# Kernel optimization log

Hardware: AMD Instinct MI355X
Metric: run time of the kernel (lower is better)

The kernel has to match this reference:

```python
import jax, jax.numpy as jnp
import numpy as np

NCLUSTERS = 256


def setup_inputs() -> dict:
    key = jax.random.key(0)
    k1, k2 = jax.random.split(key)
    pr = jax.random.normal(k1, (1024, 16384), dtype=jnp.float32)
    vr = jax.random.randint(k2, (1024, 16384, 1), 0, NCLUSTERS, dtype=jnp.int32)
    return {"pr": pr, "vr": vr}


def _group_score(pr, vr):
    nc = NCLUSTERS
    v2d = jnp.squeeze(vr, -1)            # [B, S] int cluster ids
    p = pr.reshape(-1)                   # [N]
    v = v2d.reshape(-1)                  # [N]

    # segmented mean / min / max over clusters (fused segment reduce)
    counts = jax.ops.segment_sum(jnp.ones_like(p), v, num_segments=nc)
    sums = jax.ops.segment_sum(p, v, num_segments=nc)
    vmeans = sums / counts               # empty cluster -> 0/0 = nan (matches TF)
    vmins = jax.ops.segment_min(p, v, num_segments=nc)
    vmaxs = jax.ops.segment_max(p, v, num_segments=nc)

    no_scale = vmins == vmaxs            # [nc]
    vmins_g = jnp.where(no_scale, 0.0, vmins)[v2d]   # [B, S]
    vmaxs_g = jnp.where(no_scale, 1.0, vmaxs)[v2d]   # [B, S]

    # replace nan means (empty clusters) by min(valid)/2
    nan_idx = jnp.isnan(vmeans)
    valid_min = jnp.min(jnp.where(nan_idx, jnp.inf, vmeans))
    vmeans = jnp.where(nan_idx, valid_min * 0.5, vmeans)

    # sort means, smooth with 2-tap conv, unsort
    sort_ids = jnp.argsort(vmeans)
    orig_ids = jnp.argsort(sort_ids)
    vm_s = vmeans[sort_ids]
    conv_data = jnp.concatenate([vm_s[:1], vm_s, vm_s[-1:] * 2.0])   # [nc+2]
    pair = conv_data[:-1] + conv_data[1:]                            # [nc+1]
    f0 = (pair / 1.99)[:-1]   # f0[i] = (vm_s[i-1]+vm_s[i])/1.99 (edge-padded)
    f1 = (pair / 2.01)[1:]    # f1[i] = (vm_s[i]+vm_s[i+1])/2.01, last uses 2*vm_s[-1]
    f0_g = jnp.where(no_scale, 0.0, f0[orig_ids])[v2d]  # [B, S]
    f1_g = jnp.where(no_scale, 1.0, f1[orig_ids])[v2d]  # [B, S]

    sg = jax.lax.stop_gradient
    tmp = (sg(pr) - sg(vmins_g)) / sg(vmaxs_g - vmins_g) * sg(f1_g - f0_g) + sg(f0_g)
    scale = pr / tmp
    scale = jnp.where(jnp.isnan(scale) | jnp.isinf(scale), 0.0, scale)
    return pr * sg(scale)                # [B, S]


def reference(pr, vr):
    return _group_score(pr, vr)
```

## Files before the change

### kernel.cpp

```cpp
#include <hip/hip_runtime.h>
#include <math.h>


constexpr int NC   = 256;
constexpr int TILE = 16384;


__device__ __forceinline__ unsigned int map_f(float f) {
    unsigned int u = __float_as_uint(f);
    return ((int)u < 0) ? ~u : (u | 0x80000000u);
}
__device__ __forceinline__ float unmap_f(unsigned int u) {
    return __uint_as_float((u & 0x80000000u) ? (u & 0x7FFFFFFFu) : ~u);
}

__global__ __launch_bounds__(256) void init_k(unsigned* __restrict__ g_mn,
                                              unsigned* __restrict__ g_mx) {
    g_mn[threadIdx.x] = 0xFFFFFFFFu;
    g_mx[threadIdx.x] = 0u;
}

__global__ __launch_bounds__(256) void count_k(const float* __restrict__ pr,
                                               const int* __restrict__ vr,
                                               unsigned* __restrict__ tileCnt,
                                               unsigned* __restrict__ g_mn,
                                               unsigned* __restrict__ g_mx) {
    __shared__ unsigned s_cnt[NC];
    __shared__ unsigned s_mn[NC];
    __shared__ unsigned s_mx[NC];
    const int t = blockIdx.x;
    const int tid = threadIdx.x;
    s_cnt[tid] = 0u; s_mn[tid] = 0xFFFFFFFFu; s_mx[tid] = 0u;
    __syncthreads();

    const int4*   vr4 = (const int4*)(vr) + t * (TILE / 4);
    const float4* pr4 = (const float4*)(pr) + t * (TILE / 4);
    #pragma unroll
    for (int it = 0; it < TILE / 1024; ++it) {
        int4   v = vr4[it * 256 + tid];
        float4 p = pr4[it * 256 + tid];
        int c0 = v.x & 255, c1 = v.y & 255, c2 = v.z & 255, c3 = v.w & 255;
        atomicAdd(&s_cnt[c0], 1u); atomicAdd(&s_cnt[c1], 1u);
        atomicAdd(&s_cnt[c2], 1u); atomicAdd(&s_cnt[c3], 1u);
        unsigned u0 = map_f(p.x), u1 = map_f(p.y), u2 = map_f(p.z), u3 = map_f(p.w);
        atomicMin(&s_mn[c0], u0); atomicMax(&s_mx[c0], u0);
        atomicMin(&s_mn[c1], u1); atomicMax(&s_mx[c1], u1);
        atomicMin(&s_mn[c2], u2); atomicMax(&s_mx[c2], u2);
        atomicMin(&s_mn[c3], u3); atomicMax(&s_mx[c3], u3);
    }
    __syncthreads();
    tileCnt[t * NC + tid] = s_cnt[tid];
    if (s_mn[tid] != 0xFFFFFFFFu) {
        atomicMin(&g_mn[tid], s_mn[tid]);
        atomicMax(&g_mx[tid], s_mx[tid]);
    }
}

__global__ __launch_bounds__(256) void colscan_k(unsigned* __restrict__ tileCnt,
                                                 int nt,
                                                 unsigned* __restrict__ cnt) {
    __shared__ unsigned th_sum[256];
    __shared__ unsigned ex[257];
    const int c = blockIdx.x;
    const int tid = threadIdx.x;
    const int per = nt / 256;
    unsigned loc[8];
    unsigned run = 0;
    for (int k = 0; k < per; ++k) {
        loc[k] = tileCnt[(tid * per + k) * NC + c];
        run += loc[k];
    }
    th_sum[tid] = run;
    __syncthreads();
    if (tid == 0) {
        unsigned a = 0;
        for (int j = 0; j < 256; ++j) { ex[j] = a; a += th_sum[j]; }
        ex[256] = a;
    }
    __syncthreads();
    unsigned r2 = ex[tid];
    for (int k = 0; k < per; ++k) {
        unsigned x = loc[k];
        tileCnt[(tid * per + k) * NC + c] = r2;
        r2 += x;
    }
    if (tid == 0) cnt[c] = ex[256];
}

__global__ __launch_bounds__(64) void base_k(const unsigned* __restrict__ cnt,
                                             unsigned* __restrict__ baseArr) {
    if (threadIdx.x == 0) {
        unsigned a = 0;
        for (int j = 0; j < NC; ++j) { baseArr[j] = a; a += cnt[j]; }
    }
}

__global__ __launch_bounds__(256) void scatter_k(const float* __restrict__ pr,
                                                 const int* __restrict__ vr,
                                                 const unsigned* __restrict__ tilePre,
                                                 const unsigned* __restrict__ baseArr,
                                                 float* __restrict__ srt) {
    constexpr int NW = 4;
    constexpr int QT = TILE / NW;
    __shared__ float bins[TILE];
    __shared__ unsigned whist[NW][NC];
    __shared__ unsigned wcur[NW][NC];
    __shared__ unsigned binStart[NC + 1];
    const int t = blockIdx.x;
    const int tid = threadIdx.x;
    const int w = tid >> 6, lane = tid & 63;

    for (int j = tid; j < NW * NC; j += 256) ((unsigned*)whist)[j] = 0u;
    __syncthreads();

    const int qbase = t * TILE + w * QT;
    const int4* vq4 = (const int4*)(vr + qbase);
    for (int i = lane; i < QT / 4; i += 64) {
        int4 v = vq4[i];
        atomicAdd(&whist[w][v.x & 255], 1u);
        atomicAdd(&whist[w][v.y & 255], 1u);
        atomicAdd(&whist[w][v.z & 255], 1u);
        atomicAdd(&whist[w][v.w & 255], 1u);
    }
    __syncthreads();

    {
        const int c = tid;
        unsigned off = 0;
        #pragma unroll
        for (int ww = 0; ww < NW; ++ww) {
            unsigned x = whist[ww][c];
            whist[ww][c] = off;
            off += x;
        }
        binStart[c] = off;
    }
    __syncthreads();
    if (tid == 0) {
        unsigned a = 0;
        for (int j = 0; j < NC; ++j) { unsigned x = binStart[j]; binStart[j] = a; a += x; }
        binStart[NC] = a;
    }
    __syncthreads();
    {
        const int c = tid;
        #pragma unroll
        for (int ww = 0; ww < NW; ++ww) wcur[ww][c] = binStart[c] + whist[ww][c];
    }
    __syncthreads();

    for (int g = 0; g < QT / 64; ++g) {
        int idx = qbase + g * 64 + lane;
        int v   = vr[idx] & 255;
        float p = pr[idx];
        unsigned long long m = ~0ull;
        #pragma unroll
        for (int b = 0; b < 8; ++b) {
            unsigned long long bb = __ballot((v >> b) & 1);
            m &= ((v >> b) & 1) ? bb : ~bb;
        }
        unsigned long long below = (1ull << lane) - 1ull;
        int rank   = __popcll(m & below);
        int csame  = __popcll(m);
        int leader = __ffsll((unsigned long long)m) - 1;
        unsigned base = 0;
        if (rank == 0) base = atomicAdd(&wcur[w][v], (unsigned)csame);
        base = (unsigned)__shfl((int)base, leader, 64);
        bins[base + (unsigned)rank] = p;
    }
    __syncthreads();

    for (int c = w; c < NC; c += NW) {
        unsigned s0  = binStart[c];
        unsigned len = binStart[c + 1] - s0;
        unsigned dst = baseArr[c] + tilePre[t * NC + c];
        for (unsigned i = lane; i < len; i += 64)
            srt[dst + i] = bins[s0 + i];
    }
}

__global__ __launch_bounds__(256) void chain_k(const float* __restrict__ srt,
                                               const unsigned* __restrict__ baseArr,
                                               const unsigned* __restrict__ cnt,
                                               float* __restrict__ csum) {
    constexpr unsigned CH = 8192;
    __shared__ float buf[2][CH];
    const int c = blockIdx.x;
    const unsigned b = baseArr[c];
    const unsigned n = cnt[c];
    const int tid = threadIdx.x;
    const unsigned nch = (n + CH - 1) / CH;

    {
        unsigned len0 = n < CH ? n : CH;
        const float* src = srt + b;
        for (unsigned i = tid; i < len0; i += 256) buf[0][i] = src[i];
    }
    __syncthreads();

    float s = 0.0f;
    for (unsigned ch = 0; ch < nch; ++ch) {
        const unsigned off = ch * CH;
        const unsigned len = (n - off) < CH ? (n - off) : CH;
        const unsigned nxt = off + CH;
        if (nxt < n) {
            const unsigned len2 = (n - nxt) < CH ? (n - nxt) : CH;
            const float* src = srt + b + nxt;
            float* dst = buf[(ch + 1) & 1];
            for (unsigned i = tid; i < len2; i += 256) dst[i] = src[i];
        }
        if (tid == 0) {
            const float* p = buf[ch & 1];
            const float4* p4 = (const float4*)p;
            const unsigned n4 = len >> 2;
            #pragma unroll 4
            for (unsigned i = 0; i < n4; ++i) {
                float4 x = p4[i];
                s = __fadd_rn(s, x.x);
                s = __fadd_rn(s, x.y);
                s = __fadd_rn(s, x.z);
                s = __fadd_rn(s, x.w);
            }
            for (unsigned i = n4 << 2; i < len; ++i) s = __fadd_rn(s, p[i]);
        }
        __syncthreads();
    }
    if (tid == 0) csum[c] = s;
}

__global__ __launch_bounds__(256) void finalize_k(const float* __restrict__ csum,
                                                  const unsigned* __restrict__ cnt,
                                                  const unsigned* __restrict__ g_mn,
                                                  const unsigned* __restrict__ g_mx,
                                                  float4* __restrict__ params) {
    __shared__ float vm[NC];
    __shared__ float vms[NC];
    __shared__ float s_validmin;
    const int c = threadIdx.x;

    float mean = __fdiv_rn(csum[c], (float)cnt[c]);
    vm[c] = mean;
    __syncthreads();

    if (c == 0) {
        float mn = INFINITY;
        for (int j = 0; j < NC; ++j) {
            float x = vm[j];
            if (!__builtin_isnan(x) && x < mn) mn = x;
        }
        s_validmin = mn;
    }
    __syncthreads();
    float m = vm[c];
    if (__builtin_isnan(m)) m = __fmul_rn(s_validmin, 0.5f);
    __syncthreads();
    vm[c] = m;
    __syncthreads();

    int r = 0;
    for (int j = 0; j < NC; ++j) {
        float mj = vm[j];
        r += (mj < m) || (mj == m && j < c);
    }
    vms[r] = m;
    __syncthreads();

    float mid  = vms[r];
    float left = (r == 0) ? vms[0] : vms[r - 1];
    float f0 = __fdiv_rn(__fadd_rn(left, mid), 1.99f);
    float f1 = (r == NC - 1)
                 ? __fdiv_rn(__fadd_rn(mid, __fmul_rn(mid, 2.0f)), 2.01f)
                 : __fdiv_rn(__fadd_rn(mid, vms[r + 1]), 2.01f);

    float vmin = unmap_f(g_mn[c]);
    float vmax = unmap_f(g_mx[c]);
    bool ns = (vmin == vmax);
    params[c] = ns ? make_float4(0.0f, 1.0f, 0.0f, 1.0f)
                   : make_float4(vmin, vmax, f0, f1);
}

__global__ __launch_bounds__(256) void apply_k(const float* __restrict__ pr,
                                               const int* __restrict__ vr,
                                               const float4* __restrict__ params,
                                               float* __restrict__ out, int n) {
    __shared__ float4 s_par[NC];
    for (int c = threadIdx.x; c < NC; c += blockDim.x) s_par[c] = params[c];
    __syncthreads();

    auto elem = [&](float p, int c) -> float {
        float4 par = s_par[c];
        float a   = __fsub_rn(p, par.x);
        float den = __fsub_rn(par.y, par.x);
        float q   = __fdiv_rn(a, den);
        float df  = __fsub_rn(par.w, par.z);
        float e   = __fmul_rn(q, df);
        float tmp = __fadd_rn(e, par.z);
        float scale = __fdiv_rn(p, tmp);
        if (!__builtin_isfinite(scale)) scale = 0.0f;
        return __fmul_rn(p, scale);
    };

    const int tid = blockIdx.x * blockDim.x + threadIdx.x;
    const int stride = gridDim.x * blockDim.x;
    const int n4 = n >> 2;
    const float4* pr4 = (const float4*)pr;
    const int4*   vr4 = (const int4*)vr;
    float4* out4 = (float4*)out;
    for (int i = tid; i < n4; i += stride) {
        float4 p = pr4[i];
        int4   v = vr4[i];
        float4 o;
        o.x = elem(p.x, v.x & 255);
        o.y = elem(p.y, v.y & 255);
        o.z = elem(p.z, v.z & 255);
        o.w = elem(p.w, v.w & 255);
        out4[i] = o;
    }
    for (int i = (n4 << 2) + tid; i < n; i += stride) out[i] = elem(pr[i], vr[i] & 255);
}

extern "C" void kernel_launch(void* const* d_in, const int* in_sizes, int n_in,
                              void* d_out, int out_size, void* d_ws, size_t ws_size,
                              hipStream_t stream) {
    const float* pr = (const float*)d_in[0];
    const int*   vr = (const int*)d_in[1];
    float* out = (float*)d_out;
    const int n  = in_sizes[0];
    const int nt = n / TILE;

    char* ws = (char*)d_ws;
    const size_t A = (size_t)nt * NC * 4;
    unsigned* tileCnt = (unsigned*)(ws);
    unsigned* g_cnt   = (unsigned*)(ws + A);
    unsigned* g_base  = (unsigned*)(ws + A + 1024);
    unsigned* g_mn    = (unsigned*)(ws + A + 2048);
    unsigned* g_mx    = (unsigned*)(ws + A + 3072);
    float*    g_csum  = (float*)   (ws + A + 4096);
    float4*   g_par   = (float4*)  (ws + A + 5120);

    float* srt = out;

    init_k<<<1, 256, 0, stream>>>(g_mn, g_mx);
    count_k<<<nt, 256, 0, stream>>>(pr, vr, tileCnt, g_mn, g_mx);
    colscan_k<<<NC, 256, 0, stream>>>(tileCnt, nt, g_cnt);
    base_k<<<1, 64, 0, stream>>>(g_cnt, g_base);
    scatter_k<<<nt, 256, 0, stream>>>(pr, vr, tileCnt, g_base, srt);
    chain_k<<<NC, 256, 0, stream>>>(srt, g_base, g_cnt, g_csum);
    finalize_k<<<1, 256, 0, stream>>>(g_csum, g_cnt, g_mn, g_mx, g_par);
    apply_k<<<2048, 256, 0, stream>>>(pr, vr, g_par, out, n);
}
```

Baseline: 699.6 us.

## Move per-cluster min/max into chain kernel and slim count histogram

Drops the pr read and the shared-memory atomic min/max from the counting pass, which now builds only per-wavefront histograms from vr. Per-cluster min and max are computed instead in chain_k while its loader threads copy sorted data into shared memory, using 192 loader threads so one wavefront stays free for the serial summing thread. The serial float sum is restructured to double-buffer float4 register loads so shared-memory latency overlaps the dependent adds. This removes init_k and the global atomics, but the chain kernel has fewer threads doing loads.

```diff
diff --git a/kernel.cpp b/kernel.cpp
--- a/kernel.cpp
+++ b/kernel.cpp
@@ -6,54 +6,27 @@
 constexpr int TILE = 16384;
 
 
-__device__ __forceinline__ unsigned int map_f(float f) {
-    unsigned int u = __float_as_uint(f);
-    return ((int)u < 0) ? ~u : (u | 0x80000000u);
-}
-__device__ __forceinline__ float unmap_f(unsigned int u) {
-    return __uint_as_float((u & 0x80000000u) ? (u & 0x7FFFFFFFu) : ~u);
-}
-
-__global__ __launch_bounds__(256) void init_k(unsigned* __restrict__ g_mn,
-                                              unsigned* __restrict__ g_mx) {
-    g_mn[threadIdx.x] = 0xFFFFFFFFu;
-    g_mx[threadIdx.x] = 0u;
-}
-
-__global__ __launch_bounds__(256) void count_k(const float* __restrict__ pr,
-                                               const int* __restrict__ vr,
-                                               unsigned* __restrict__ tileCnt,
-                                               unsigned* __restrict__ g_mn,
-                                               unsigned* __restrict__ g_mx) {
-    __shared__ unsigned s_cnt[NC];
-    __shared__ unsigned s_mn[NC];
-    __shared__ unsigned s_mx[NC];
+__global__ __launch_bounds__(256) void count_k(const int* __restrict__ vr,
+                                               unsigned* __restrict__ tileCnt) {
+    constexpr int NW = 4;
+    __shared__ unsigned whist[NW][NC];
     const int t = blockIdx.x;
     const int tid = threadIdx.x;
-    s_cnt[tid] = 0u; s_mn[tid] = 0xFFFFFFFFu; s_mx[tid] = 0u;
-    __syncthreads();
-
-    const int4*   vr4 = (const int4*)(vr) + t * (TILE / 4);
-    const float4* pr4 = (const float4*)(pr) + t * (TILE / 4);
-    #pragma unroll
-    for (int it = 0; it < TILE / 1024; ++it) {
-        int4   v = vr4[it * 256 + tid];
-        float4 p = pr4[it * 256 + tid];
-        int c0 = v.x & 255, c1 = v.y & 255, c2 = v.z & 255, c3 = v.w & 255;
-        atomicAdd(&s_cnt[c0], 1u); atomicAdd(&s_cnt[c1], 1u);
-        atomicAdd(&s_cnt[c2], 1u); atomicAdd(&s_cnt[c3], 1u);
-        unsigned u0 = map_f(p.x), u1 = map_f(p.y), u2 = map_f(p.z), u3 = map_f(p.w);
-        atomicMin(&s_mn[c0], u0); atomicMax(&s_mx[c0], u0);
-        atomicMin(&s_mn[c1], u1); atomicMax(&s_mx[c1], u1);
-        atomicMin(&s_mn[c2], u2); atomicMax(&s_mx[c2], u2);
-        atomicMin(&s_mn[c3], u3); atomicMax(&s_mx[c3], u3);
-    }
-    __syncthreads();
-    tileCnt[t * NC + tid] = s_cnt[tid];
-    if (s_mn[tid] != 0xFFFFFFFFu) {
-        atomicMin(&g_mn[tid], s_mn[tid]);
-        atomicMax(&g_mx[tid], s_mx[tid]);
-    }
+    const int w = tid >> 6, lane = tid & 63;
+    for (int j = tid; j < NW * NC; j += 256) ((unsigned*)whist)[j] = 0u;
+    __syncthreads();
+
+    const int qbase = t * TILE + w * (TILE / NW);
+    const int4* vq4 = (const int4*)(vr + qbase);
+    for (int i = lane; i < TILE / NW / 4; i += 64) {
+        int4 v = vq4[i];
+        atomicAdd(&whist[w][v.x & 255], 1u);
+        atomicAdd(&whist[w][v.y & 255], 1u);
+        atomicAdd(&whist[w][v.z & 255], 1u);
+        atomicAdd(&whist[w][v.w & 255], 1u);
+    }
+    __syncthreads();
+    tileCnt[t * NC + tid] = whist[0][tid] + whist[1][tid] + whist[2][tid] + whist[3][tid];
 }
 
 __global__ __launch_bounds__(256) void colscan_k(unsigned* __restrict__ tileCnt,
@@ -182,19 +155,29 @@
 __global__ __launch_bounds__(256) void chain_k(const float* __restrict__ srt,
                                                const unsigned* __restrict__ baseArr,
                                                const unsigned* __restrict__ cnt,
-                                               float* __restrict__ csum) {
+                                               float* __restrict__ csum,
+                                               float* __restrict__ vmnF,
+                                               float* __restrict__ vmxF) {
     constexpr unsigned CH = 8192;
     __shared__ float buf[2][CH];
+    __shared__ float redmn[256];
+    __shared__ float redmx[256];
     const int c = blockIdx.x;
     const unsigned b = baseArr[c];
     const unsigned n = cnt[c];
     const int tid = threadIdx.x;
     const unsigned nch = (n + CH - 1) / CH;
 
-    {
-        unsigned len0 = n < CH ? n : CH;
+    float lmn = INFINITY, lmx = -INFINITY;
+
+    if (tid >= 64) {
+        const unsigned len0 = n < CH ? n : CH;
         const float* src = srt + b;
-        for (unsigned i = tid; i < len0; i += 256) buf[0][i] = src[i];
+        for (unsigned i = (unsigned)(tid - 64); i < len0; i += 192) {
+            float x = src[i];
+            buf[0][i] = x;
+            lmn = fminf(lmn, x); lmx = fmaxf(lmx, x);
+        }
     }
     __syncthreads();
 
@@ -203,35 +186,68 @@
         const unsigned off = ch * CH;
         const unsigned len = (n - off) < CH ? (n - off) : CH;
         const unsigned nxt = off + CH;
-        if (nxt < n) {
+        if (tid >= 64 && nxt < n) {
             const unsigned len2 = (n - nxt) < CH ? (n - nxt) : CH;
             const float* src = srt + b + nxt;
             float* dst = buf[(ch + 1) & 1];
-            for (unsigned i = tid; i < len2; i += 256) dst[i] = src[i];
+            for (unsigned i = (unsigned)(tid - 64); i < len2; i += 192) {
+                float x = src[i];
+                dst[i] = x;
+                lmn = fminf(lmn, x); lmx = fmaxf(lmx, x);
+            }
         }
         if (tid == 0) {
             const float* p = buf[ch & 1];
             const float4* p4 = (const float4*)p;
-            const unsigned n4 = len >> 2;
-            #pragma unroll 4
-            for (unsigned i = 0; i < n4; ++i) {
-                float4 x = p4[i];
-                s = __fadd_rn(s, x.x);
-                s = __fadd_rn(s, x.y);
-                s = __fadd_rn(s, x.z);
-                s = __fadd_rn(s, x.w);
+            const unsigned ng = len >> 5;
+            float4 A[8], B[8];
+            auto LOAD8 = [&](float4 (&R)[8], unsigned g) {
+                const float4* q = p4 + g * 8;
+                #pragma unroll
+                for (int k = 0; k < 8; ++k) R[k] = q[k];
+            };
+            auto ADD8 = [&](const float4 (&R)[8]) {
+                #pragma unroll
+                for (int k = 0; k < 8; ++k) {
+                    s = __fadd_rn(s, R[k].x); s = __fadd_rn(s, R[k].y);
+                    s = __fadd_rn(s, R[k].z); s = __fadd_rn(s, R[k].w);
+                }
+            };
+            unsigned g = 0;
+            if (ng) {
+                LOAD8(A, 0);
+                for (; g + 2 < ng; g += 2) {
+                    LOAD8(B, g + 1);
+                    ADD8(A);
+                    LOAD8(A, g + 2);
+                    ADD8(B);
+                }
+                if (g + 1 < ng) { LOAD8(B, g + 1); ADD8(A); ADD8(B); g += 2; }
+                else            { ADD8(A); g += 1; }
             }
-            for (unsigned i = n4 << 2; i < len; ++i) s = __fadd_rn(s, p[i]);
+            for (unsigned i = g << 5; i < len; ++i) s = __fadd_rn(s, p[i]);
         }
         __syncthreads();
     }
-    if (tid == 0) csum[c] = s;
+
+    redmn[tid] = lmn; redmx[tid] = lmx;
+    __syncthreads();
+    if (tid == 0) {
+        float mn = INFINITY, mx = -INFINITY;
+        for (int j = 64; j < 256; ++j) {
+            mn = fminf(mn, redmn[j]);
+            mx = fmaxf(mx, redmx[j]);
+        }
+        csum[c] = s;
+        vmnF[c] = mn;
+        vmxF[c] = mx;
+    }
 }
 
 __global__ __launch_bounds__(256) void finalize_k(const float* __restrict__ csum,
                                                   const unsigned* __restrict__ cnt,
-                                                  const unsigned* __restrict__ g_mn,
-                                                  const unsigned* __restrict__ g_mx,
+                                                  const float* __restrict__ vmnF,
+                                                  const float* __restrict__ vmxF,
                                                   float4* __restrict__ params) {
     __shared__ float vm[NC];
     __shared__ float vms[NC];
@@ -272,8 +288,8 @@
                  ? __fdiv_rn(__fadd_rn(mid, __fmul_rn(mid, 2.0f)), 2.01f)
                  : __fdiv_rn(__fadd_rn(mid, vms[r + 1]), 2.01f);
 
-    float vmin = unmap_f(g_mn[c]);
-    float vmax = unmap_f(g_mx[c]);
+    float vmin = vmnF[c];
+    float vmax = vmxF[c];
     bool ns = (vmin == vmax);
     params[c] = ns ? make_float4(0.0f, 1.0f, 0.0f, 1.0f)
                    : make_float4(vmin, vmax, f0, f1);
@@ -333,19 +349,18 @@
     unsigned* tileCnt = (unsigned*)(ws);
     unsigned* g_cnt   = (unsigned*)(ws + A);
     unsigned* g_base  = (unsigned*)(ws + A + 1024);
-    unsigned* g_mn    = (unsigned*)(ws + A + 2048);
-    unsigned* g_mx    = (unsigned*)(ws + A + 3072);
+    float*    g_vmn   = (float*)   (ws + A + 2048);
+    float*    g_vmx   = (float*)   (ws + A + 3072);
     float*    g_csum  = (float*)   (ws + A + 4096);
     float4*   g_par   = (float4*)  (ws + A + 5120);
 
     float* srt = out;
 
-    init_k<<<1, 256, 0, stream>>>(g_mn, g_mx);
-    count_k<<<nt, 256, 0, stream>>>(pr, vr, tileCnt, g_mn, g_mx);
+    count_k<<<nt, 256, 0, stream>>>(vr, tileCnt);
     colscan_k<<<NC, 256, 0, stream>>>(tileCnt, nt, g_cnt);
     base_k<<<1, 64, 0, stream>>>(g_cnt, g_base);
     scatter_k<<<nt, 256, 0, stream>>>(pr, vr, tileCnt, g_base, srt);
-    chain_k<<<NC, 256, 0, stream>>>(srt, g_base, g_cnt, g_csum);
-    finalize_k<<<1, 256, 0, stream>>>(g_csum, g_cnt, g_mn, g_mx, g_par);
+    chain_k<<<NC, 256, 0, stream>>>(srt, g_base, g_cnt, g_csum, g_vmn, g_vmx);
+    finalize_k<<<1, 256, 0, stream>>>(g_csum, g_cnt, g_vmn, g_vmx, g_par);
     apply_k<<<2048, 256, 0, stream>>>(pr, vr, g_par, out, n);
 }
```

Result: faster. 585.6 us (-16.3%).
